# Kernel tuning notes

Measured on AMD Instinct MI355X. Metric: run time of the kernel, lower is better.

The kernel has to match this reference:

```python
import jax, jax.numpy as jnp
import numpy as np
from jax import lax

SLOPE = 0.01  # nn.LeakyReLU default negative slope

def leaky(x):
    return jnp.where(x >= 0, x, SLOPE * x)

def conv2d(x, w, b, pad):
    # x: [N,C,H,W], w: [O,I,kh,kw]
    y = lax.conv_general_dilated(x, w, (1, 1), [(pad, pad), (pad, pad)],
                                 dimension_numbers=('NCHW', 'OIHW', 'NCHW'))
    return y + b[None, :, None, None]

def centered_ifftn(x, axes):
    # np.fft.fftshift(np.fft.ifftn(np.fft.ifftshift(X), norm='ortho'))
    return jnp.fft.fftshift(jnp.fft.ifftn(jnp.fft.ifftshift(x, axes=axes), axes=axes, norm='ortho'), axes=axes)

def setup_inputs() -> dict:
    key = jax.random.key(0)
    ks = jax.random.split(key, 10)
    B, H, W, CK = 8, 640, 368, 32
    return {
        'img':    jax.random.normal(ks[0], (B, 1, H, W), jnp.float32),
        'kspace': jax.random.normal(ks[1], (B, 2, H, W), jnp.float32),
        # k_model1: Conv2d(2, CK, 3, padding=1) + LeakyReLU
        'wk': jax.random.normal(ks[2], (CK, 2, 3, 3), jnp.float32) * 0.1,
        'bk': jnp.zeros((CK,), jnp.float32),
        # conv1: Conv2d(CK, 2, kernel_size=1)
        'w1': jax.random.normal(ks[3], (2, CK, 1, 1), jnp.float32) * 0.1,
        'b1': jnp.zeros((2,), jnp.float32),
        # conv2: Conv2d(2, 1, kernel_size=1)
        'w2': jax.random.normal(ks[4], (1, 2, 1, 1), jnp.float32) * 0.1,
        'b2': jnp.zeros((1,), jnp.float32),
        # i_model1: Conv2d(1, 1, 3, padding=1) + LeakyReLU
        'wi': jax.random.normal(ks[5], (1, 1, 3, 3), jnp.float32) * 0.1,
        'bi': jnp.zeros((1,), jnp.float32),
    }

def reference(img, kspace, wk, bk, w1, b1, w2, b2, wi, bi):
    # k-space branch: k_model1 then conv1 + LeakyReLU
    out1 = leaky(conv2d(leaky(conv2d(kspace, wk, bk, 1)), w1, b1, 0))  # [B,2,H,W]
    # channel 0 = real, channel 1 = imag; ifftn over ALL axes (incl. batch),
    # exactly as the original numpy call with axes=range(out.ndim)
    cplx = out1[:, 0].astype(jnp.complex64) + 1j * out1[:, 1].astype(jnp.complex64)  # [B,H,W]
    im = jnp.abs(centered_ifftn(cplx, (0, 1, 2)))[:, None]  # [B,1,H,W]
    # concat with image, cast to half (torch.cuda.HalfTensor), conv2 + LeakyReLU
    out = jnp.concatenate([im, img], axis=1).astype(jnp.float16)  # [B,2,H,W]
    out = leaky(conv2d(out, w2.astype(jnp.float16), b2.astype(jnp.float16), 0))
    out = out.astype(jnp.float32)  # [B,1,H,W]
    # image-domain model
    return leaky(conv2d(out, wi, bi, 1))  # [B,1,H,W]
```

## Files before the change

kernel.cpp:

```cpp
#include <hip/hip_runtime.h>
#include <hip/hip_fp16.h>
#include <math.h>

#define B_ 8
#define H_ 640
#define W_ 368
#define HW_ (H_*W_)
#define NP_ (B_*H_*W_)

#define FROWS 4
#define HLINES 4
#define HP 645
#define TS 16

typedef __attribute__((ext_vector_type(8))) short v8s;
typedef __attribute__((ext_vector_type(4))) float v4f;

__device__ __forceinline__ float leaky_(float x){ return fmaxf(x, 0.01f*x); }

__device__ __forceinline__ unsigned short f2bf(float x){
    unsigned u = __float_as_uint(x);
    u += 0x7FFFu + ((u >> 16) & 1u);
    return (unsigned short)(u >> 16);
}

__device__ __forceinline__ float2 cadd_(float2 a, float2 b){ return make_float2(a.x+b.x, a.y+b.y); }
__device__ __forceinline__ float2 csub_(float2 a, float2 b){ return make_float2(a.x-b.x, a.y-b.y); }
__device__ __forceinline__ float2 cmul_(float2 a, float c, float s){
    return make_float2(a.x*c - a.y*s, a.x*s + a.y*c);
}
__device__ __forceinline__ float2 cmulv_(float2 a, float2 w){
    return make_float2(a.x*w.x - a.y*w.y, a.x*w.y + a.y*w.x);
}

__device__ __forceinline__ void dft4p_(float2 p0, float2 p1, float2 p2, float2 p3,
                                       float2& z0, float2& z1, float2& z2, float2& z3){
    float2 s0 = cadd_(p0,p2), d0 = csub_(p0,p2);
    float2 s1 = cadd_(p1,p3), d1 = csub_(p1,p3);
    z0 = cadd_(s0,s1);
    z2 = csub_(s0,s1);
    z1 = make_float2(d0.x - d1.y, d0.y + d1.x);
    z3 = make_float2(d0.x + d1.y, d0.y - d1.x);
}

__device__ __forceinline__ void fft16p_(const float2* x, float2* X){
    const float C1 = 0.9238795325112867f, S1 = 0.3826834323650898f;
    const float R  = 0.7071067811865476f;
    float2 Y[4][4];
    #pragma unroll
    for (int b = 0; b < 4; ++b)
        dft4p_(x[b], x[4+b], x[8+b], x[12+b], Y[b][0], Y[b][1], Y[b][2], Y[b][3]);
    Y[1][1] = cmul_(Y[1][1],  C1,  S1);
    Y[1][2] = cmul_(Y[1][2],   R,   R);
    Y[1][3] = cmul_(Y[1][3],  S1,  C1);
    Y[2][1] = cmul_(Y[2][1],   R,   R);
    Y[2][2] = make_float2(-Y[2][2].y, Y[2][2].x);
    Y[2][3] = cmul_(Y[2][3],  -R,   R);
    Y[3][1] = cmul_(Y[3][1],  S1,  C1);
    Y[3][2] = cmul_(Y[3][2],  -R,   R);
    Y[3][3] = cmul_(Y[3][3], -C1, -S1);
    #pragma unroll
    for (int c = 0; c < 4; ++c)
        dft4p_(Y[0][c], Y[1][c], Y[2][c], Y[3][c], X[c], X[c+4], X[c+8], X[c+12]);
}

__device__ __forceinline__ void fft8p_(const float2* x, float2* X){
    const float R = 0.7071067811865476f;
    float2 Y0[4], Y1[4];
    dft4p_(x[0], x[2], x[4], x[6], Y0[0], Y0[1], Y0[2], Y0[3]);
    dft4p_(x[1], x[3], x[5], x[7], Y1[0], Y1[1], Y1[2], Y1[3]);
    float2 T0 = Y1[0];
    float2 T1 = cmul_(Y1[1],  R, R);
    float2 T2 = make_float2(-Y1[2].y, Y1[2].x);
    float2 T3 = cmul_(Y1[3], -R, R);
    X[0] = cadd_(Y0[0], T0);  X[4] = csub_(Y0[0], T0);
    X[1] = cadd_(Y0[1], T1);  X[5] = csub_(Y0[1], T1);
    X[2] = cadd_(Y0[2], T2);  X[6] = csub_(Y0[2], T2);
    X[3] = cadd_(Y0[3], T3);  X[7] = csub_(Y0[3], T3);
}

__global__ void init_tables_kernel(float2* __restrict__ T){
    int i = blockIdx.x*blockDim.x + threadIdx.x;
    if (i >= 1301) return;
    int r, c, modN; int j;
    if      (i <  368){ j = i;        r = j%16; c = j/16; modN = 368; }
    else if (i < 1008){ j = i-368;    r = j%16; c = j/16; modN = 640; }
    else if (i < 1048){ j = i-1008;   r = j%8;  c = j/8;  modN = 40;  }
    else              { j = i-1048;   r = j/11; c = j%11 + 1; modN = 23; }
    int t = (int)(((long long)r * c) % modN);
    if (t > modN/2) t -= modN;
    float ang = (float)(6.283185307179586 * ((double)t / (double)modN));
    float s, co;
    sincosf(ang, &s, &co);
    T[i] = make_float2(co, s);
}

__global__ __launch_bounds__(256) void kfftw_kernel(const float* __restrict__ ksp,
                               const float* __restrict__ wk,
                               const float* __restrict__ bk,
                               const float* __restrict__ w1,
                               const float* __restrict__ b1,
                               const float2* __restrict__ TW368P,
                               const float2* __restrict__ F23P,
                               float2* __restrict__ Bt){
    __shared__ unsigned short Sb[4836];
    __shared__ unsigned short Wr[4*512];
    __shared__ float2 X[FROWS*369];
    int t = threadIdx.x;
    int blk = blockIdx.x;
    int b  = blk / 160;
    int h0 = (blk - b*160) * FROWS;

    for (int seg = 0; seg < 12; ++seg){
        int r = seg >> 1, ic = seg & 1;
        int hh = h0 - 1 + r;
        int ok = ((unsigned)hh < 640u);
        const float* base = ksp + ((size_t)(b*2 + ic)*640 + (ok ? hh : 0))*368;
        for (int col = t; col < 372; col += 256){
            int c = col - 1;
            float v = (ok && (unsigned)c < 368u) ? base[c] : 0.f;
            Sb[seg*372 + col] = f2bf(v);
        }
    }
    for (int i = t; i < 372; i += 256) Sb[4464 + i] = 0;

    int lane = t & 63, wave = t >> 6;
    int oc = lane & 15, q = lane >> 4;
    int l = wave;

    int off[8];
    v8s bf0, bf1, b2f;
    #pragma unroll
    for (int j = 0; j < 8; ++j){
        int kk = q*8 + j;
        if (kk < 18){
            int ic = (kk >= 9) ? 1 : 0;
            int tt = kk - ic*9;
            int ty = tt/3, tx = tt - ty*3;
            off[j] = ((ty + l)*2 + ic)*372 + tx;
            bf0[j] = (short)f2bf(wk[oc*18 + kk]);
            bf1[j] = (short)f2bf(wk[(oc+16)*18 + kk]);
        } else {
            off[j] = 4464;
            bf0[j] = 0; bf1[j] = 0;
        }
        b2f[j] = (oc < 2) ? (short)f2bf(w1[oc*32 + kk]) : (short)0;
    }
    float bk0 = bk[oc], bk1 = bk[oc+16];
    float biasn = (oc == 1) ? b1[1] : b1[0];
    unsigned short* Wrw = Wr + (wave << 9);
    __syncthreads();

    for (int g = 0; g < 23; ++g){
        int w0m = g*16 + oc;
        v8s af;
        #pragma unroll
        for (int j = 0; j < 8; ++j) af[j] = (short)Sb[off[j] + w0m];
        v4f d0 = {0.f,0.f,0.f,0.f}, d1 = {0.f,0.f,0.f,0.f};
        d0 = __builtin_amdgcn_mfma_f32_16x16x32_bf16(af, bf0, d0, 0, 0, 0);
        d1 = __builtin_amdgcn_mfma_f32_16x16x32_bf16(af, bf1, d1, 0, 0, 0);
        #pragma unroll
        for (int r = 0; r < 4; ++r){
            int px = q*4 + r;
            Wrw[px*32 + oc]      = f2bf(leaky_(d0[r] + bk0));
            Wrw[px*32 + 16 + oc] = f2bf(leaky_(d1[r] + bk1));
        }
        asm volatile("s_waitcnt lgkmcnt(0)" ::: "memory");
        const v8s* ap = (const v8s*)(Wrw + oc*32);
        v8s a2 = ap[q];
        v4f d2 = {0.f,0.f,0.f,0.f};
        d2 = __builtin_amdgcn_mfma_f32_16x16x32_bf16(a2, b2f, d2, 0, 0, 0);
        float vals[4], ov[4];
        #pragma unroll
        for (int r = 0; r < 4; ++r){
            vals[r] = leaky_(biasn + d2[r]);
            ov[r] = __shfl_xor(vals[r], 1);
        }
        if (oc == 0){
            int px = g*16 + q*4;
            X[l*369 + px  ] = make_float2( vals[0],  ov[0]);
            X[l*369 + px+1] = make_float2(-vals[1], -ov[1]);
            X[l*369 + px+2] = make_float2( vals[2],  ov[2]);
            X[l*369 + px+3] = make_float2(-vals[3], -ov[3]);
        }
        asm volatile("s_waitcnt lgkmcnt(0)" ::: "memory");
    }
    __syncthreads();

    if (t < 92){
        int ll = t & 3, n2 = t >> 2;
        float2 xr[16], Xo[16];
        #pragma unroll
        for (int n1 = 0; n1 < 16; ++n1) xr[n1] = X[ll*369 + 23*n1 + n2];
        fft16p_(xr, Xo);
        const float2* row = TW368P + n2*16;
        #pragma unroll
        for (int k1 = 0; k1 < 16; ++k1)
            X[ll*369 + 23*k1 + n2] = cmulv_(Xo[k1], row[k1]);
    }
    __syncthreads();

    {
        int ll = t & 3, k1 = (t >> 2) & 15, qr = t >> 6;
        const float2* xp = X + ll*369 + 23*k1;
        float2 x0 = xp[0];
        float2 u[11], d[11];
        #pragma unroll
        for (int m = 1; m <= 11; ++m){
            float2 a = xp[m], bb = xp[23-m];
            u[m-1] = cadd_(a, bb);
            d[m-1] = csub_(a, bb);
        }
        __syncthreads();
        int k2beg = qr*6;
        int k2end = (qr == 3) ? 23 : k2beg + 6;
        for (int k2 = k2beg; k2 < k2end; ++k2){
            const float2* row = F23P + k2*11;
            float re = x0.x, im = x0.y;
            #pragma unroll
            for (int m = 0; m < 11; ++m){
                float c = row[m].x, s = row[m].y;
                re += u[m].x*c - d[m].y*s;
                im += u[m].y*c + d[m].x*s;
            }
            X[ll*369 + k1 + 16*k2] = make_float2(re, im);
        }
    }
    __syncthreads();

    const float sc = 0.052129458158616354f;
    for (int i = t; i < FROWS*368; i += 256){
        int k = i >> 2, ll = i & 3;
        float2 v = X[ll*369 + k];
        float s = (k & 1) ? -sc : sc;
        Bt[((size_t)(b*368 + k))*640 + h0 + ll] = make_float2(v.x*s, v.y*s);
    }
}

__global__ __launch_bounds__(256) void fftH_kernel(const float2* __restrict__ Bt,
                                                   const float2* __restrict__ TW640P,
                                                   const float2* __restrict__ TW40P,
                                                   float2* __restrict__ A2){
    __shared__ float2 X[HLINES*HP];
    int t = threadIdx.x;
    size_t base = (size_t)blockIdx.x * (HLINES*640);

    for (int i = t; i < HLINES*640; i += 256){
        int l = i / 640, n = i - l*640;
        float2 v = Bt[base + i];
        float s = (n & 1) ? -1.f : 1.f;
        X[l*HP + n] = make_float2(v.x*s, v.y*s);
    }
    __syncthreads();

    if (t < 160){
        int l = t & 3, n2 = t >> 2;
        float2 xr[16], Xo[16];
        #pragma unroll
        for (int n1 = 0; n1 < 16; ++n1) xr[n1] = X[l*HP + 40*n1 + n2];
        fft16p_(xr, Xo);
        const float2* row = TW640P + n2*16;
        #pragma unroll
        for (int k1 = 0; k1 < 16; ++k1)
            X[l*HP + 40*k1 + n2] = cmulv_(Xo[k1], row[k1]);
    }
    __syncthreads();

    for (int it = t; it < 320; it += 256){
        int l = it & 3, k1 = (it >> 2) & 15, m2 = it >> 6;
        float2 xr[8], Xo[8];
        #pragma unroll
        for (int m1 = 0; m1 < 8; ++m1) xr[m1] = X[l*HP + 40*k1 + 5*m1 + m2];
        fft8p_(xr, Xo);
        const float2* row = TW40P + m2*8;
        #pragma unroll
        for (int j1 = 0; j1 < 8; ++j1)
            X[l*HP + 40*k1 + 5*j1 + m2] = cmulv_(Xo[j1], row[j1]);
    }
    __syncthreads();

    {
        const float CK1[5] = {1.f,  0.30901699437494745f, -0.8090169943749475f, -0.8090169943749475f,  0.30901699437494745f};
        const float SK1[5] = {0.f,  0.9510565162951535f,   0.5877852522924731f, -0.5877852522924731f, -0.9510565162951535f};
        const float CK2[5] = {1.f, -0.8090169943749475f,   0.30901699437494745f, 0.30901699437494745f, -0.8090169943749475f};
        const float SK2[5] = {0.f,  0.5877852522924731f,  -0.9510565162951535f,  0.9510565162951535f, -0.5877852522924731f};
        int it0 = t, it1 = t + 256;
        int l0 = it0 & 3, k10 = (it0 >> 2) & 15, j10 = it0 >> 6;
        int l1 = it1 & 3, k11 = (it1 >> 2) & 15, j11 = it1 >> 6;
        float2 p0[5], p1[5];
        #pragma unroll
        for (int m2 = 0; m2 < 5; ++m2) p0[m2] = X[l0*HP + 40*k10 + 5*j10 + m2];
        #pragma unroll
        for (int m2 = 0; m2 < 5; ++m2) p1[m2] = X[l1*HP + 40*k11 + 5*j11 + m2];
        __syncthreads();
        float2 u0a = cadd_(p0[1], p0[4]), d0a = csub_(p0[1], p0[4]);
        float2 u0b = cadd_(p0[2], p0[3]), d0b = csub_(p0[2], p0[3]);
        float2 u1a = cadd_(p1[1], p1[4]), d1a = csub_(p1[1], p1[4]);
        float2 u1b = cadd_(p1[2], p1[3]), d1b = csub_(p1[2], p1[3]);
        #pragma unroll
        for (int j2 = 0; j2 < 5; ++j2){
            float c1v = CK1[j2], s1v = SK1[j2], c2v = CK2[j2], s2v = SK2[j2];
            float re0 = p0[0].x + u0a.x*c1v - d0a.y*s1v + u0b.x*c2v - d0b.y*s2v;
            float im0 = p0[0].y + u0a.y*c1v + d0a.x*s1v + u0b.y*c2v + d0b.x*s2v;
            float re1 = p1[0].x + u1a.x*c1v - d1a.y*s1v + u1b.x*c2v - d1b.y*s2v;
            float im1 = p1[0].y + u1a.y*c1v + d1a.x*s1v + u1b.y*c2v + d1b.x*s2v;
            X[l0*HP + k10 + 16*j10 + 128*j2] = make_float2(re0, im0);
            X[l1*HP + k11 + 16*j11 + 128*j2] = make_float2(re1, im1);
        }
    }
    __syncthreads();

    const float sc = 0.03952847075210474f;
    for (int i = t; i < HLINES*640; i += 256){
        int l = i / 640, k = i - l*640;
        float2 v = X[l*HP + k];
        float s = (k & 1) ? -sc : sc;
        A2[base + i] = make_float2(v.x*s, v.y*s);
    }
}

__global__ __launch_bounds__(256) void tail_kernel(const float2* __restrict__ A2,
                                  const float* __restrict__ img,
                                  const float* __restrict__ w2,
                                  const float* __restrict__ b2,
                                  const float* __restrict__ wi,
                                  const float* __restrict__ bi,
                                  float* __restrict__ out){
    __shared__ float Pl[8][TS+2][TS+3];
    int t = threadIdx.x;
    int ty0 = (blockIdx.x / 23) * TS;
    int tx0 = (blockIdx.x % 23) * TS;

    float w2h0 = __half2float(__float2half(w2[0]));
    float w2h1 = __half2float(__float2half(w2[1]));
    float b2h  = __half2float(__float2half(b2[0]));
    const float sc8 = 0.35355339059327373f;

    for (int idx = t; idx < (TS+2)*(TS+2); idx += 256){
        int hx = idx / (TS+2), hy = idx - hx*(TS+2);
        int hh = ty0 - 1 + hy, ww = tx0 - 1 + hx;
        int hc = min(max(hh, 0), H_-1), wc = min(max(ww, 0), W_-1);
        float2 x[8], Xo[8];
        #pragma unroll
        for (int n = 0; n < 8; ++n){
            float2 v = A2[((size_t)(n*368 + wc))*640 + hc];
            float s = (n & 1) ? -1.f : 1.f;
            x[n] = make_float2(v.x*s, v.y*s);
        }
        fft8p_(x, Xo);
        #pragma unroll
        for (int k = 0; k < 8; ++k){
            float s = (k & 1) ? -sc8 : sc8;
            float yr = Xo[k].x * s, yi = Xo[k].y * s;
            float mag = sqrtf(yr*yr + yi*yi);
            Pl[k][hy][hx] = __half2float(__float2half(mag));
        }
    }
    __syncthreads();

    for (int idx = t; idx < (TS+2)*(TS+2); idx += 256){
        int hy = idx / (TS+2), hx = idx - hy*(TS+2);
        int hh = ty0 - 1 + hy, ww = tx0 - 1 + hx;
        bool inb = (hh >= 0) && (hh < H_) && (ww >= 0) && (ww < W_);
        int hc = min(max(hh, 0), H_-1), wc = min(max(ww, 0), W_-1);
        float inbf = inb ? 1.f : 0.f;
        #pragma unroll
        for (int k = 0; k < 8; ++k){
            float g = __half2float(__float2half(img[(size_t)k*HW_ + hc*W_ + wc]));
            float a = Pl[k][hy][hx];
            float o = leaky_(a*w2h0 + g*w2h1 + b2h);
            o = __half2float(__float2half(o));
            Pl[k][hy][hx] = o * inbf;
        }
    }
    __syncthreads();

    int sy = t >> 4, sx = t & 15;
    float wv[9];
    #pragma unroll
    for (int q = 0; q < 9; ++q) wv[q] = wi[q];
    float bi0 = bi[0];
    #pragma unroll
    for (int k = 0; k < 8; ++k){
        float acc = bi0;
        #pragma unroll
        for (int dy = 0; dy < 3; ++dy)
            #pragma unroll
            for (int dx = 0; dx < 3; ++dx)
                acc += wv[dy*3+dx] * Pl[k][sy+dy][sx+dx];
        out[((size_t)k*H_ + ty0+sy)*W_ + tx0+sx] = leaky_(acc);
    }
}

extern "C" void kernel_launch(void* const* d_in, const int* in_sizes, int n_in,
                              void* d_out, int out_size, void* d_ws, size_t ws_size,
                              hipStream_t stream){
    const float* img = (const float*)d_in[0];
    const float* ksp = (const float*)d_in[1];
    const float* wk  = (const float*)d_in[2];
    const float* bk  = (const float*)d_in[3];
    const float* w1  = (const float*)d_in[4];
    const float* b1  = (const float*)d_in[5];
    const float* w2  = (const float*)d_in[6];
    const float* b2  = (const float*)d_in[7];
    const float* wi  = (const float*)d_in[8];
    const float* bi  = (const float*)d_in[9];

    char* ws = (char*)d_ws;
    float2* Bt  = (float2*)(ws + 0);
    float2* A2  = (float2*)(ws + 15073280);
    float2* T   = (float2*)(ws + 30146560);
    float2* TW368P = T + 0;
    float2* TW640P = T + 368;
    float2* TW40P  = T + 1008;
    float2* F23P   = T + 1048;
    float* out  = (float*)d_out;

    init_tables_kernel<<<6, 256, 0, stream>>>(T);

    kfftw_kernel<<<B_*(H_/FROWS), 256, 0, stream>>>(ksp, wk, bk, w1, b1,
                                                    TW368P, F23P, Bt);
    fftH_kernel<<<(B_*W_)/HLINES, 256, 0, stream>>>(Bt, TW640P, TW40P, A2);
    tail_kernel<<<(H_/TS)*(W_/TS), 256, 0, stream>>>(A2, img, w2, b2, wi, bi, out);
}
```

Before: 171.4 us.

## Chain conv MFMAs through register shuffles instead of LDS round-trip

Swaps the MFMA operand order so the first conv's output lands in a layout that can be repacked with cross-lane shuffles. That output then feeds the 1x1 conv MFMA directly, with no LDS scratch write/read and no waitcnt stalls. Biases are folded into the accumulator init and bf16 packing uses v_cvt_pk_bf16_f32. The zero-padding region of shared memory is removed and padded taps are masked in registers. In exchange it adds extra shuffles and selects per group and depends on the MFMA lane layout being exactly right.

```diff
diff --git a/kernel.cpp b/kernel.cpp
--- a/kernel.cpp
+++ b/kernel.cpp
@@ -22,6 +22,12 @@
     unsigned u = __float_as_uint(x);
     u += 0x7FFFu + ((u >> 16) & 1u);
     return (unsigned short)(u >> 16);
+}
+
+__device__ __forceinline__ unsigned cvtpk_(float lo, float hi){
+    unsigned r;
+    asm("v_cvt_pk_bf16_f32 %0, %1, %2" : "=v"(r) : "v"(lo), "v"(hi));
+    return r;
 }
 
 __device__ __forceinline__ float2 cadd_(float2 a, float2 b){ return make_float2(a.x+b.x, a.y+b.y); }
@@ -103,8 +109,7 @@
                                const float2* __restrict__ TW368P,
                                const float2* __restrict__ F23P,
                                float2* __restrict__ Bt){
-    __shared__ unsigned short Sb[4836];
-    __shared__ unsigned short Wr[4*512];
+    __shared__ unsigned short Sb[4464];
     __shared__ float2 X[FROWS*369];
     int t = threadIdx.x;
     int blk = blockIdx.x;
@@ -122,7 +127,6 @@
             Sb[seg*372 + col] = f2bf(v);
         }
     }
-    for (int i = t; i < 372; i += 256) Sb[4464 + i] = 0;
 
     int lane = t & 63, wave = t >> 6;
     int oc = lane & 15, q = lane >> 4;
@@ -141,49 +145,61 @@
             bf0[j] = (short)f2bf(wk[oc*18 + kk]);
             bf1[j] = (short)f2bf(wk[(oc+16)*18 + kk]);
         } else {
-            off[j] = 4464;
+            off[j] = 0;
             bf0[j] = 0; bf1[j] = 0;
         }
         b2f[j] = (oc < 2) ? (short)f2bf(w1[oc*32 + kk]) : (short)0;
     }
-    float bk0 = bk[oc], bk1 = bk[oc+16];
+    float bkA[4], bkB[4];
+    #pragma unroll
+    for (int r = 0; r < 4; ++r){
+        bkA[r] = bk[q*4 + r];
+        bkB[r] = bk[16 + q*4 + r];
+    }
     float biasn = (oc == 1) ? b1[1] : b1[0];
-    unsigned short* Wrw = Wr + (wave << 9);
+    bool qis0 = (q == 0), qis1 = (q == 1), qis2 = (q == 2);
+    bool qhi  = (q & 2) != 0;
+    float* Xf = (float*)X;
     __syncthreads();
 
     for (int g = 0; g < 23; ++g){
         int w0m = g*16 + oc;
         v8s af;
         #pragma unroll
-        for (int j = 0; j < 8; ++j) af[j] = (short)Sb[off[j] + w0m];
-        v4f d0 = {0.f,0.f,0.f,0.f}, d1 = {0.f,0.f,0.f,0.f};
-        d0 = __builtin_amdgcn_mfma_f32_16x16x32_bf16(af, bf0, d0, 0, 0, 0);
-        d1 = __builtin_amdgcn_mfma_f32_16x16x32_bf16(af, bf1, d1, 0, 0, 0);
-        #pragma unroll
-        for (int r = 0; r < 4; ++r){
-            int px = q*4 + r;
-            Wrw[px*32 + oc]      = f2bf(leaky_(d0[r] + bk0));
-            Wrw[px*32 + 16 + oc] = f2bf(leaky_(d1[r] + bk1));
-        }
-        asm volatile("s_waitcnt lgkmcnt(0)" ::: "memory");
-        const v8s* ap = (const v8s*)(Wrw + oc*32);
-        v8s a2 = ap[q];
-        v4f d2 = {0.f,0.f,0.f,0.f};
-        d2 = __builtin_amdgcn_mfma_f32_16x16x32_bf16(a2, b2f, d2, 0, 0, 0);
-        float vals[4], ov[4];
-        #pragma unroll
-        for (int r = 0; r < 4; ++r){
-            vals[r] = leaky_(biasn + d2[r]);
-            ov[r] = __shfl_xor(vals[r], 1);
-        }
-        if (oc == 0){
-            int px = g*16 + q*4;
-            X[l*369 + px  ] = make_float2( vals[0],  ov[0]);
-            X[l*369 + px+1] = make_float2(-vals[1], -ov[1]);
-            X[l*369 + px+2] = make_float2( vals[2],  ov[2]);
-            X[l*369 + px+3] = make_float2(-vals[3], -ov[3]);
-        }
-        asm volatile("s_waitcnt lgkmcnt(0)" ::: "memory");
+        for (int j = 0; j < 8; ++j){
+            short v = 0;
+            if (q*8 + j < 18) v = (short)Sb[off[j] + w0m];
+            af[j] = v;
+        }
+        v4f d0 = {bkA[0], bkA[1], bkA[2], bkA[3]};
+        v4f d1 = {bkB[0], bkB[1], bkB[2], bkB[3]};
+        d0 = __builtin_amdgcn_mfma_f32_16x16x32_bf16(bf0, af, d0, 0, 0, 0);
+        d1 = __builtin_amdgcn_mfma_f32_16x16x32_bf16(bf1, af, d1, 0, 0, 0);
+        unsigned p0 = cvtpk_(leaky_(d0[0]), leaky_(d0[1]));
+        unsigned p1 = cvtpk_(leaky_(d0[2]), leaky_(d0[3]));
+        unsigned p2 = cvtpk_(leaky_(d1[0]), leaky_(d1[1]));
+        unsigned p3 = cvtpk_(leaky_(d1[2]), leaky_(d1[3]));
+        unsigned vSa = qhi ? p2 : p0, vSb = qhi ? p3 : p1;
+        unsigned vTa = qhi ? p0 : p2, vTb = qhi ? p1 : p3;
+        unsigned X16a = __shfl_xor(vSa, 16), X16b = __shfl_xor(vSb, 16);
+        unsigned X32a = __shfl_xor(vTa, 32), X32b = __shfl_xor(vTb, 32);
+        unsigned X48a = __shfl_xor(vTa, 48), X48b = __shfl_xor(vTb, 48);
+        unsigned m0 = qis0 ? p0   : (qis1 ? X48a : (qis2 ? X32a : X16a));
+        unsigned m1 = qis0 ? p1   : (qis1 ? X48b : (qis2 ? X32b : X16b));
+        unsigned m2 = qis0 ? X16a : (qis1 ? X32a : (qis2 ? X48a : p2));
+        unsigned m3 = qis0 ? X16b : (qis1 ? X32b : (qis2 ? X48b : p3));
+        union { unsigned u[4]; v8s s; } uu;
+        uu.u[0] = m0; uu.u[1] = m1; uu.u[2] = m2; uu.u[3] = m3;
+        v4f d2 = {biasn, biasn, biasn, biasn};
+        d2 = __builtin_amdgcn_mfma_f32_16x16x32_bf16(uu.s, b2f, d2, 0, 0, 0);
+        if (oc < 2){
+            #pragma unroll
+            for (int r = 0; r < 4; ++r){
+                int px = g*16 + q*4 + r;
+                float s = (r & 1) ? -1.f : 1.f;
+                Xf[(l*369 + px)*2 + oc] = s * leaky_(d2[r]);
+            }
+        }
     }
     __syncthreads();
 
```

New measurement: 186.9 us. +9.0%, slower.

## Switch k-space conv to 32x32x16 MFMA and do 1x1 conv in registers

Applied to the files above, without the earlier changes.

Recomputes the 3x3 conv (2->32 channels) with a 32x32x16 bf16 MFMA. Channels go on the M dimension and 32 pixels on N. The bias is folded in through a constant-one column in a second MFMA. The 1x1 conv (32->2) now runs as per-lane FMAs plus a cross-half shuffle, replacing the LDS round-trip and the third MFMA. This removes the Wr shared buffer and its waitcnt barriers and cuts the loop from 23 to 12 iterations. In exchange it adds 32 more registers per thread and does the 1x1 reduction in fp32, not bf16.

```diff
diff --git a/kernel.cpp b/kernel.cpp
--- a/kernel.cpp
+++ b/kernel.cpp
@@ -15,6 +15,7 @@
 
 typedef __attribute__((ext_vector_type(8))) short v8s;
 typedef __attribute__((ext_vector_type(4))) float v4f;
+typedef __attribute__((ext_vector_type(16))) float v16f;
 
 __device__ __forceinline__ float leaky_(float x){ return fmaxf(x, 0.01f*x); }
 
@@ -104,7 +105,6 @@
                                const float2* __restrict__ F23P,
                                float2* __restrict__ Bt){
     __shared__ unsigned short Sb[4836];
-    __shared__ unsigned short Wr[4*512];
     __shared__ float2 X[FROWS*369];
     int t = threadIdx.x;
     int blk = blockIdx.x;
@@ -125,65 +125,66 @@
     for (int i = t; i < 372; i += 256) Sb[4464 + i] = 0;
 
     int lane = t & 63, wave = t >> 6;
-    int oc = lane & 15, q = lane >> 4;
+    int ch = lane & 31, h = lane >> 5;
     int l = wave;
 
-    int off[8];
-    v8s bf0, bf1, b2f;
+    int offB[8];
+    v8s a1, a2;
     #pragma unroll
     for (int j = 0; j < 8; ++j){
-        int kk = q*8 + j;
-        if (kk < 18){
-            int ic = (kk >= 9) ? 1 : 0;
-            int tt = kk - ic*9;
-            int ty = tt/3, tx = tt - ty*3;
-            off[j] = ((ty + l)*2 + ic)*372 + tx;
-            bf0[j] = (short)f2bf(wk[oc*18 + kk]);
-            bf1[j] = (short)f2bf(wk[(oc+16)*18 + kk]);
-        } else {
-            off[j] = 4464;
-            bf0[j] = 0; bf1[j] = 0;
-        }
-        b2f[j] = (oc < 2) ? (short)f2bf(w1[oc*32 + kk]) : (short)0;
-    }
-    float bk0 = bk[oc], bk1 = bk[oc+16];
-    float biasn = (oc == 1) ? b1[1] : b1[0];
-    unsigned short* Wrw = Wr + (wave << 9);
-    __syncthreads();
-
-    for (int g = 0; g < 23; ++g){
-        int w0m = g*16 + oc;
-        v8s af;
-        #pragma unroll
-        for (int j = 0; j < 8; ++j) af[j] = (short)Sb[off[j] + w0m];
-        v4f d0 = {0.f,0.f,0.f,0.f}, d1 = {0.f,0.f,0.f,0.f};
-        d0 = __builtin_amdgcn_mfma_f32_16x16x32_bf16(af, bf0, d0, 0, 0, 0);
-        d1 = __builtin_amdgcn_mfma_f32_16x16x32_bf16(af, bf1, d1, 0, 0, 0);
-        #pragma unroll
-        for (int r = 0; r < 4; ++r){
-            int px = q*4 + r;
-            Wrw[px*32 + oc]      = f2bf(leaky_(d0[r] + bk0));
-            Wrw[px*32 + 16 + oc] = f2bf(leaky_(d1[r] + bk1));
-        }
-        asm volatile("s_waitcnt lgkmcnt(0)" ::: "memory");
-        const v8s* ap = (const v8s*)(Wrw + oc*32);
-        v8s a2 = ap[q];
-        v4f d2 = {0.f,0.f,0.f,0.f};
-        d2 = __builtin_amdgcn_mfma_f32_16x16x32_bf16(a2, b2f, d2, 0, 0, 0);
-        float vals[4], ov[4];
-        #pragma unroll
-        for (int r = 0; r < 4; ++r){
-            vals[r] = leaky_(biasn + d2[r]);
-            ov[r] = __shfl_xor(vals[r], 1);
-        }
-        if (oc == 0){
-            int px = g*16 + q*4;
-            X[l*369 + px  ] = make_float2( vals[0],  ov[0]);
-            X[l*369 + px+1] = make_float2(-vals[1], -ov[1]);
-            X[l*369 + px+2] = make_float2( vals[2],  ov[2]);
-            X[l*369 + px+3] = make_float2(-vals[3], -ov[3]);
-        }
-        asm volatile("s_waitcnt lgkmcnt(0)" ::: "memory");
+        int kk = 8*h + j;
+        int ic = (kk >= 9) ? 1 : 0;
+        int tt = kk - ic*9;
+        int ty = tt/3, tx = tt - ty*3;
+        offB[j] = ((ty + l)*2 + ic)*372 + tx;
+        a1[j] = (short)f2bf(wk[ch*18 + kk]);
+        a2[j] = 0;
+    }
+    if (h == 0){
+        a2[0] = (short)f2bf(wk[ch*18 + 16]);
+        a2[1] = (short)f2bf(wk[ch*18 + 17]);
+        a2[2] = (short)f2bf(bk[ch]);
+    }
+    const int off16 = ((2 + l)*2 + 1)*372 + 1;
+    const int off17 = off16 + 1;
+
+    float wp0[16], wp1[16];
+    #pragma unroll
+    for (int r = 0; r < 16; ++r){
+        int row = (r & 3) + 8*(r >> 2) + 4*h;
+        wp0[r] = w1[row];
+        wp1[r] = w1[32 + row];
+    }
+    float b10 = b1[0], b11 = b1[1];
+    float sgn = (ch & 1) ? -1.f : 1.f;
+    __syncthreads();
+
+    for (int g = 0; g < 12; ++g){
+        int px = g*32 + ch;
+        v8s bv;
+        #pragma unroll
+        for (int j = 0; j < 8; ++j) bv[j] = (short)Sb[offB[j] + px];
+        v16f d = {0.f,0.f,0.f,0.f,0.f,0.f,0.f,0.f,0.f,0.f,0.f,0.f,0.f,0.f,0.f,0.f};
+        d = __builtin_amdgcn_mfma_f32_32x32x16_bf16(a1, bv, d, 0, 0, 0);
+        v8s b2v = {0,0,0,0,0,0,0,0};
+        b2v[0] = (short)Sb[off16 + px];
+        b2v[1] = (short)Sb[off17 + px];
+        b2v[2] = (short)0x3F80;
+        d = __builtin_amdgcn_mfma_f32_32x32x16_bf16(a2, b2v, d, 0, 0, 0);
+        float sx = 0.f, sy = 0.f;
+        #pragma unroll
+        for (int r = 0; r < 16; ++r){
+            float y = leaky_(d[r]);
+            sx = fmaf(y, wp0[r], sx);
+            sy = fmaf(y, wp1[r], sy);
+        }
+        sx += __shfl_xor(sx, 32);
+        sy += __shfl_xor(sy, 32);
+        if (h == 0 && px < 368){
+            float o0 = leaky_(sx + b10);
+            float o1 = leaky_(sy + b11);
+            X[l*369 + px] = make_float2(sgn*o0, sgn*o1);
+        }
     }
     __syncthreads();
 
```

Measured after the change: 155.6 us. 1.1x faster.
